# Performance work log

Measured on AMD Instinct MI355X. Metric: run time of the kernel, lower is better.

## Reference

```python
import jax, jax.numpy as jnp
import numpy as np

S = 4096
V = 50000
E = 512
H = 512
CE = 128
CH = 128
T = 50


def _lstm_dir(x, W_ih, W_hh, b, reverse):
    # x: [S, D]; PyTorch gate order i, f, g, o. b = b_ih + b_hh fused.
    gx = x @ W_ih.T + b  # [S, 4H] precomputed input contribution
    Hd = W_hh.shape[1]
    def step(carry, g_t):
        h, c = carry
        g = g_t + h @ W_hh.T
        i, f, gg, o = jnp.split(g, 4, axis=-1)
        c = jax.nn.sigmoid(f) * c + jax.nn.sigmoid(i) * jnp.tanh(gg)
        h = jax.nn.sigmoid(o) * jnp.tanh(c)
        return (h, c), h
    init = (jnp.zeros((Hd,), x.dtype), jnp.zeros((Hd,), x.dtype))
    _, hs = jax.lax.scan(step, init, gx, reverse=reverse)
    return hs  # [S, H]


def _bilstm(x, Wih_f, Whh_f, b_f, Wih_b, Whh_b, b_b):
    fwd = _lstm_dir(x, Wih_f, Whh_f, b_f, False)
    bwd = _lstm_dir(x, Wih_b, Whh_b, b_b, True)
    return jnp.concatenate([fwd, bwd], axis=-1)  # [S, 2H]


def _viterbi(emissions, start_t, end_t, trans):
    # emissions: [S, T]. Standard CRF Viterbi (torchcrf semantics).
    score0 = start_t + emissions[0]  # [T]
    def step(score, emit):
        m = score[:, None] + trans          # [T_prev, T_cur]
        bp = jnp.argmax(m, axis=0)          # best previous tag for each cur tag
        new_score = jnp.max(m, axis=0) + emit
        return new_score, bp
    final, bps = jax.lax.scan(step, score0, emissions[1:])  # bps: [S-1, T]
    final = final + end_t
    last = jnp.argmax(final)
    def back(tag, bp):
        prev = bp[tag]
        return prev, prev
    _, path_head = jax.lax.scan(back, last, bps, reverse=True)  # [S-1]
    return jnp.concatenate([path_head, last[None]])  # [S]


def setup_inputs() -> dict:
    key = jax.random.key(0)
    ks = jax.random.split(key, 20)
    s = 0.05
    inp = {
        'sentence': jax.random.randint(ks[0], (S,), 0, V),
        'char_sentence': jax.random.randint(ks[1], (S,), 0, V),
        'word_emb': jax.random.normal(ks[2], (V, E), jnp.float32) * s,
        'char_emb': jax.random.normal(ks[3], (V, CE), jnp.float32) * s,
        # char BiLSTM
        'cWih_f': jax.random.normal(ks[4], (4 * CH, CE), jnp.float32) * s,
        'cWhh_f': jax.random.normal(ks[5], (4 * CH, CH), jnp.float32) * s,
        'cb_f': jnp.zeros((4 * CH,), jnp.float32),
        'cWih_b': jax.random.normal(ks[6], (4 * CH, CE), jnp.float32) * s,
        'cWhh_b': jax.random.normal(ks[7], (4 * CH, CH), jnp.float32) * s,
        'cb_b': jnp.zeros((4 * CH,), jnp.float32),
        # word BiLSTM (input dim E + 2*CH)
        'wWih_f': jax.random.normal(ks[8], (4 * H, E + 2 * CH), jnp.float32) * s,
        'wWhh_f': jax.random.normal(ks[9], (4 * H, H), jnp.float32) * s,
        'wb_f': jnp.zeros((4 * H,), jnp.float32),
        'wWih_b': jax.random.normal(ks[10], (4 * H, E + 2 * CH), jnp.float32) * s,
        'wWhh_b': jax.random.normal(ks[11], (4 * H, H), jnp.float32) * s,
        'wb_b': jnp.zeros((4 * H,), jnp.float32),
        # hidden2tag
        'W_tag': jax.random.normal(ks[12], (T, 2 * H), jnp.float32) * s,
        'b_tag': jnp.zeros((T,), jnp.float32),
        # CRF params
        'start_t': jax.random.normal(ks[13], (T,), jnp.float32) * s,
        'end_t': jax.random.normal(ks[14], (T,), jnp.float32) * s,
        'trans': jax.random.normal(ks[15], (T, T), jnp.float32) * s,
    }
    return inp


def reference(sentence, char_sentence, word_emb, char_emb,
              cWih_f, cWhh_f, cb_f, cWih_b, cWhh_b, cb_b,
              wWih_f, wWhh_f, wb_f, wWih_b, wWhh_b, wb_b,
              W_tag, b_tag, start_t, end_t, trans):
    we = word_emb[sentence]          # [S, E]
    ce = char_emb[char_sentence]     # [S, CE]
    char_out = _bilstm(ce, cWih_f, cWhh_f, cb_f, cWih_b, cWhh_b, cb_b)  # [S, 2*CH]
    emb = jnp.concatenate([we, char_out], axis=-1)  # [S, E + 2*CH]
    lstm_out = _bilstm(emb, wWih_f, wWhh_f, wb_f, wWih_b, wWhh_b, wb_b)  # [S, 2H]
    tag_space = lstm_out @ W_tag.T + b_tag  # [S, T] emissions
    path = _viterbi(tag_space, start_t, end_t, trans)  # [S] int32 tags
    return path
```

## Files before the change

### kernel.cpp

```cpp
#include <hip/hip_runtime.h>
#include <math.h>

#define SQ   4096
#define EDIM 512
#define CEDIM 128
#define CHH  128
#define WH   512
#define NT   50

typedef unsigned long long ull;

__device__ __forceinline__ float sigf(float x) { return 1.0f / (1.0f + expf(-x)); }

#define PIN4(V) asm volatile("" : "+v"(V.x), "+v"(V.y), "+v"(V.z), "+v"(V.w));

__device__ __forceinline__ void ld8x_sc0(const ull* p, ull& q0, ull& q1, ull& q2,
                                         ull& q3, ull& q4, ull& q5, ull& q6, ull& q7) {
    asm volatile("global_load_dwordx2 %0, %8, off sc0\n\t"
                 "global_load_dwordx2 %1, %8, off offset:8 sc0\n\t"
                 "global_load_dwordx2 %2, %8, off offset:16 sc0\n\t"
                 "global_load_dwordx2 %3, %8, off offset:24 sc0\n\t"
                 "global_load_dwordx2 %4, %8, off offset:32 sc0\n\t"
                 "global_load_dwordx2 %5, %8, off offset:40 sc0\n\t"
                 "global_load_dwordx2 %6, %8, off offset:48 sc0\n\t"
                 "global_load_dwordx2 %7, %8, off offset:56 sc0\n\t"
                 "s_waitcnt vmcnt(0)"
                 : "=&v"(q0), "=&v"(q1), "=&v"(q2), "=&v"(q3),
                   "=&v"(q4), "=&v"(q5), "=&v"(q6), "=&v"(q7)
                 : "v"(p) : "memory");
}
__device__ __forceinline__ ull ld_mir(const ull* p) {
    return __hip_atomic_load(p, __ATOMIC_RELAXED, __HIP_MEMORY_SCOPE_AGENT);
}
__device__ __forceinline__ void st_plain8(ull* p, ull v) {
    asm volatile("global_store_dwordx2 %0, %1, off" :: "v"(p), "v"(v) : "memory");
}
__device__ __forceinline__ void st_mir(ull* p, ull v) {
    __hip_atomic_store(p, v, __ATOMIC_RELAXED, __HIP_MEMORY_SCOPE_AGENT);
}
__device__ __forceinline__ unsigned umin2(unsigned a, unsigned b) { return a < b ? a : b; }

#define FMA4(W, off) { float4 h4 = *(const float4*)&hc[off]; \
    a0 += W.x * h4.x; a1 += W.y * h4.y; a2 += W.z * h4.z; a3 += W.w * h4.w; }

#define CW(n) float4 w##n = wp[n]; PIN4(w##n)

__global__ __launch_bounds__(256) void k1_gather_cgx(
    const int* __restrict__ sent, const int* __restrict__ csent,
    const float* __restrict__ wemb, const float* __restrict__ cemb,
    const float* __restrict__ cWih_f, const float* __restrict__ cb_f,
    const float* __restrict__ cWih_b, const float* __restrict__ cb_b,
    float* __restrict__ we_g, float* __restrict__ cgx)
{
    const int tid = threadIdx.x;
    const int t0 = blockIdx.x * 16;
    __shared__ __align__(16) float ceL[16][128];
    __shared__ int sids[16], cids[16];
    if (tid < 16) sids[tid] = sent[t0 + tid];
    else if (tid < 32) cids[tid - 16] = csent[t0 + tid - 16];
    __syncthreads();
    {
        int f4 = tid;
        for (int q = 0; q < 2; ++q, f4 += 256) {
            int r = f4 >> 5, k4 = f4 & 31;
            float4 v = *(const float4*)&cemb[(size_t)cids[r] * CEDIM + k4 * 4];
            *(float4*)&ceL[r][k4 * 4] = v;
        }
    }
    {
        int f4 = tid;
        for (int q = 0; q < 8; ++q, f4 += 256) {
            int r = f4 >> 7, k4 = f4 & 127;
            float4 v = *(const float4*)&wemb[(size_t)sids[r] * EDIM + k4 * 4];
            *(float4*)&we_g[(size_t)(t0 + r) * EDIM + k4 * 4] = v;
        }
    }
    __syncthreads();
    for (int q = 0; q < 4; ++q) {
        int j = q * 256 + tid;
        int d = j >> 9, r = j & 511;
        const float* Wih = d ? cWih_b : cWih_f;
        const float* cb = d ? cb_b : cb_f;
        float b = cb[r];
        float acc[16];
#pragma unroll
        for (int tt = 0; tt < 16; ++tt) acc[tt] = b;
        for (int k4 = 0; k4 < 32; ++k4) {
            float4 wv = *(const float4*)&Wih[r * CEDIM + k4 * 4];
#pragma unroll
            for (int tt = 0; tt < 16; ++tt) {
                acc[tt] += wv.x * ceL[tt][k4 * 4 + 0] + wv.y * ceL[tt][k4 * 4 + 1]
                         + wv.z * ceL[tt][k4 * 4 + 2] + wv.w * ceL[tt][k4 * 4 + 3];
            }
        }
#pragma unroll
        for (int tt = 0; tt < 16; ++tt)
            cgx[((size_t)d * SQ + (t0 + tt)) * 512 + r] = acc[tt];
    }
}

__global__ __launch_bounds__(512, 2) void k2_charlstm_gemm(
    const float* __restrict__ cWhh_f, const float* __restrict__ cWhh_b,
    const float* __restrict__ cgx, float* __restrict__ cho,
    const float* __restrict__ we_g,
    const float* __restrict__ wWih_f, const float* __restrict__ wb_f,
    const float* __restrict__ wWih_b, const float* __restrict__ wb_b,
    float* __restrict__ wgx)
{
    const int tid = threadIdx.x;
    __shared__ __align__(16) float At[32][68];
    __shared__ __align__(16) float Bt[32][128];
    __shared__ __align__(16) float hstC[128];
    __shared__ float gb[512];

    if (blockIdx.x < 2) {
        const int dir = blockIdx.x;
        const float* Whh = dir ? cWhh_b : cWhh_f;
        const int row = tid;
        const float4* wp = (const float4*)&Whh[(size_t)row * CHH];
        CW(0)  CW(1)  CW(2)  CW(3)  CW(4)  CW(5)  CW(6)  CW(7)
        CW(8)  CW(9)  CW(10) CW(11) CW(12) CW(13) CW(14) CW(15)
        CW(16) CW(17) CW(18) CW(19) CW(20) CW(21) CW(22) CW(23)
        CW(24) CW(25) CW(26) CW(27) CW(28) CW(29) CW(30) CW(31)

        const float* gxc = cgx + (size_t)dir * SQ * 512;
        float cst = 0.f;
        float gxp0 = gxc[(size_t)(dir ? (SQ - 1) : 0) * 512 + row];
        float gxp1 = gxc[(size_t)(dir ? (SQ - 2) : 1) * 512 + row];
        if (tid < 32) *(float4*)&hstC[tid * 4] = make_float4(0, 0, 0, 0);
        __syncthreads();
        for (int t = 0; t < SQ; ++t) {
            const int x = dir ? (SQ - 1 - t) : t;
            float gxv = gxp0;
            gxp0 = gxp1;
            if (t + 2 < SQ) {
                const int x2 = dir ? (SQ - 3 - t) : (t + 2);
                gxp1 = gxc[(size_t)x2 * 512 + row];
            }
            float a0 = 0.f, a1 = 0.f, a2 = 0.f, a3 = 0.f;
            const float* hc = hstC;
            FMA4(w0, 0)    FMA4(w1, 4)    FMA4(w2, 8)    FMA4(w3, 12)
            FMA4(w4, 16)   FMA4(w5, 20)   FMA4(w6, 24)   FMA4(w7, 28)
            FMA4(w8, 32)   FMA4(w9, 36)   FMA4(w10, 40)  FMA4(w11, 44)
            FMA4(w12, 48)  FMA4(w13, 52)  FMA4(w14, 56)  FMA4(w15, 60)
            FMA4(w16, 64)  FMA4(w17, 68)  FMA4(w18, 72)  FMA4(w19, 76)
            FMA4(w20, 80)  FMA4(w21, 84)  FMA4(w22, 88)  FMA4(w23, 92)
            FMA4(w24, 96)  FMA4(w25, 100) FMA4(w26, 104) FMA4(w27, 108)
            FMA4(w28, 112) FMA4(w29, 116) FMA4(w30, 120) FMA4(w31, 124)
            gb[row] = (a0 + a1) + (a2 + a3) + gxv;
            __syncthreads();
            if (tid < 128) {
                float siv = gb[tid], sfv = gb[128 + tid];
                float sgv = gb[256 + tid], sov = gb[384 + tid];
                float iv = sigf(siv), fv = sigf(sfv), ov = sigf(sov);
                float yg = sigf(sgv + sgv);
                float gv = yg + yg - 1.f;
                cst = fv * cst + iv * gv;
                float ts = sigf(cst + cst);
                float h = ov * (ts + ts - 1.f);
                hstC[tid] = h;
                cho[(size_t)x * 256 + dir * CHH + tid] = h;
            }
            __syncthreads();
        }
        return;
    }
    const int tile = blockIdx.x - 2;
    const int dir = tile >> 10;
    const int rem = tile & 1023;
    const int mb = rem >> 4;
    const int nb = rem & 15;
    const float* Wih = dir ? wWih_b : wWih_f;
    const float* wb = dir ? wb_b : wb_f;
    float* C = wgx + (size_t)dir * SQ * 2048;
    const int tm = tid >> 5, tn = tid & 31;
    float acc[4][4];
#pragma unroll
    for (int i = 0; i < 4; ++i)
#pragma unroll
        for (int jj = 0; jj < 4; ++jj) acc[i][jj] = 0.f;
    for (int kb = 0; kb < 16; ++kb) {
        {
            int rowm = tid >> 3, k4 = tid & 7;
            float4 v = *(const float4*)&we_g[(size_t)(mb * 64 + rowm) * EDIM + kb * 32 + k4 * 4];
            At[k4 * 4 + 0][rowm] = v.x; At[k4 * 4 + 1][rowm] = v.y;
            At[k4 * 4 + 2][rowm] = v.z; At[k4 * 4 + 3][rowm] = v.w;
        }
#pragma unroll
        for (int q = 0; q < 2; ++q) {
            int f4 = q * 512 + tid;
            int rr = f4 >> 3, k4 = f4 & 7;
            float4 v = *(const float4*)&Wih[(size_t)(nb * 128 + rr) * 768 + kb * 32 + k4 * 4];
            Bt[k4 * 4 + 0][rr] = v.x; Bt[k4 * 4 + 1][rr] = v.y;
            Bt[k4 * 4 + 2][rr] = v.z; Bt[k4 * 4 + 3][rr] = v.w;
        }
        __syncthreads();
#pragma unroll
        for (int kk = 0; kk < 32; ++kk) {
            float4 a4 = *(const float4*)&At[kk][tm * 4];
            float4 b4 = *(const float4*)&Bt[kk][tn * 4];
            acc[0][0] += a4.x * b4.x; acc[0][1] += a4.x * b4.y; acc[0][2] += a4.x * b4.z; acc[0][3] += a4.x * b4.w;
            acc[1][0] += a4.y * b4.x; acc[1][1] += a4.y * b4.y; acc[1][2] += a4.y * b4.z; acc[1][3] += a4.y * b4.w;
            acc[2][0] += a4.z * b4.x; acc[2][1] += a4.z * b4.y; acc[2][2] += a4.z * b4.z; acc[2][3] += a4.z * b4.w;
            acc[3][0] += a4.w * b4.x; acc[3][1] += a4.w * b4.y; acc[3][2] += a4.w * b4.z; acc[3][3] += a4.w * b4.w;
        }
        __syncthreads();
    }
    float4 wbv = *(const float4*)&wb[nb * 128 + tn * 4];
#pragma unroll
    for (int i = 0; i < 4; ++i) {
        float4 o;
        o.x = acc[i][0] + wbv.x; o.y = acc[i][1] + wbv.y;
        o.z = acc[i][2] + wbv.z; o.w = acc[i][3] + wbv.w;
        *(float4*)&C[(size_t)(mb * 64 + tm * 4 + i) * 2048 + nb * 128 + tn * 4] = o;
    }
}

__global__ __launch_bounds__(512, 2) void k3_gemm_char(
    const float* __restrict__ cho,
    const float* __restrict__ wWih_f, const float* __restrict__ wWih_b,
    float* __restrict__ wgx)
{
    const int tid = threadIdx.x;
    const int tile = blockIdx.x;
    const int dir = tile >> 10;
    const int rem = tile & 1023;
    const int mb = rem >> 4, nb = rem & 15;
    const float* Wih = dir ? wWih_b : wWih_f;
    float* C = wgx + (size_t)dir * SQ * 2048;
    __shared__ __align__(16) float At[32][68];
    __shared__ __align__(16) float Bt[32][128];
    const int tm = tid >> 5, tn = tid & 31;
    float acc[4][4];
#pragma unroll
    for (int i = 0; i < 4; ++i)
#pragma unroll
        for (int jj = 0; jj < 4; ++jj) acc[i][jj] = 0.f;
    for (int kb = 0; kb < 8; ++kb) {
        {
            int rowm = tid >> 3, k4 = tid & 7;
            float4 v = *(const float4*)&cho[(size_t)(mb * 64 + rowm) * 256 + kb * 32 + k4 * 4];
            At[k4 * 4 + 0][rowm] = v.x; At[k4 * 4 + 1][rowm] = v.y;
            At[k4 * 4 + 2][rowm] = v.z; At[k4 * 4 + 3][rowm] = v.w;
        }
#pragma unroll
        for (int q = 0; q < 2; ++q) {
            int f4 = q * 512 + tid;
            int rr = f4 >> 3, k4 = f4 & 7;
            float4 v = *(const float4*)&Wih[(size_t)(nb * 128 + rr) * 768 + 512 + kb * 32 + k4 * 4];
            Bt[k4 * 4 + 0][rr] = v.x; Bt[k4 * 4 + 1][rr] = v.y;
            Bt[k4 * 4 + 2][rr] = v.z; Bt[k4 * 4 + 3][rr] = v.w;
        }
        __syncthreads();
#pragma unroll
        for (int kk = 0; kk < 32; ++kk) {
            float4 a4 = *(const float4*)&At[kk][tm * 4];
            float4 b4 = *(const float4*)&Bt[kk][tn * 4];
            acc[0][0] += a4.x * b4.x; acc[0][1] += a4.x * b4.y; acc[0][2] += a4.x * b4.z; acc[0][3] += a4.x * b4.w;
            acc[1][0] += a4.y * b4.x; acc[1][1] += a4.y * b4.y; acc[1][2] += a4.y * b4.z; acc[1][3] += a4.y * b4.w;
            acc[2][0] += a4.z * b4.x; acc[2][1] += a4.z * b4.y; acc[2][2] += a4.z * b4.z; acc[2][3] += a4.z * b4.w;
            acc[3][0] += a4.w * b4.x; acc[3][1] += a4.w * b4.y; acc[3][2] += a4.w * b4.z; acc[3][3] += a4.w * b4.w;
        }
        __syncthreads();
    }
#pragma unroll
    for (int i = 0; i < 4; ++i) {
        float* cp = &C[(size_t)(mb * 64 + tm * 4 + i) * 2048 + nb * 128 + tn * 4];
        float4 o = *(float4*)cp;
        o.x += acc[i][0]; o.y += acc[i][1]; o.z += acc[i][2]; o.w += acc[i][3];
        *(float4*)cp = o;
    }
}

__global__ __launch_bounds__(1024, 4) void k4_word_lstm(
    const float* __restrict__ wWhh_f, const float* __restrict__ wWhh_b,
    const float* __restrict__ wgx, float* __restrict__ lstm, ull* __restrict__ pairs)
{
    const int res = blockIdx.x & 7;
    if (res > 1) return;
    const int dir = res;
    const int wid = blockIdx.x >> 3;
    const int tid = threadIdx.x;
    const int k = tid >> 6;
    const int r = tid & 63;
    const int g = r >> 4, u = r & 15;
    const float* Whh = dir ? wWhh_b : wWhh_f;
    const int G = g * WH + wid * 16 + u;
    const float4* wp = (const float4*)&Whh[(size_t)G * WH + k * 32];
    float4 w0 = wp[0], w1 = wp[1], w2 = wp[2], w3 = wp[3];
    float4 w4 = wp[4], w5 = wp[5], w6 = wp[6], w7 = wp[7];
    PIN4(w0) PIN4(w1) PIN4(w2) PIN4(w3) PIN4(w4) PIN4(w5) PIN4(w6) PIN4(w7)

    __shared__ __align__(16) float hst[512];
    __shared__ float part[16][65];

    ull* wpf = pairs;
    ull* wpm = pairs + 2048;
    const float* gx = wgx + (size_t)dir * SQ * 2048;
    float cst = 0.f;
    int useFast = 1, alive = 1;
    for (int t = 0; t < SQ; ++t) {
        const int x = dir ? (SQ - 1 - t) : t;
        float gxv = 0.f;
        if (tid < 64)
            gxv = gx[(size_t)x * 2048 + (size_t)(tid >> 4) * 512 + wid * 16 + (tid & 15)];
        if (t == 0) {
            if (tid < 128) *(float4*)&hst[tid * 4] = make_float4(0, 0, 0, 0);
        } else if (tid < 64) {
            const size_t boff = ((size_t)((t - 1) & 1) * 2 + dir) * 512 + tid * 8;
            const ull* pf = wpf + boff;
            const ull* pm = wpm + boff;
            ull q0 = 0, q1 = 0, q2 = 0, q3 = 0, q4 = 0, q5 = 0, q6 = 0, q7 = 0;
            int spins = 0;
            while (alive) {
                if (useFast) {
                    ld8x_sc0(pf, q0, q1, q2, q3, q4, q5, q6, q7);
                } else {
                    q0 = ld_mir(pm + 0); q1 = ld_mir(pm + 1);
                    q2 = ld_mir(pm + 2); q3 = ld_mir(pm + 3);
                    q4 = ld_mir(pm + 4); q5 = ld_mir(pm + 5);
                    q6 = ld_mir(pm + 6); q7 = ld_mir(pm + 7);
                }
                unsigned tm = umin2(umin2(umin2((unsigned)(q0 >> 32), (unsigned)(q1 >> 32)),
                                          umin2((unsigned)(q2 >> 32), (unsigned)(q3 >> 32))),
                                    umin2(umin2((unsigned)(q4 >> 32), (unsigned)(q5 >> 32)),
                                          umin2((unsigned)(q6 >> 32), (unsigned)(q7 >> 32))));
                if (__all(tm >= (unsigned)t)) break;
                ++spins;
                if (useFast && spins > 2048) { useFast = 0; spins = 0; }
                if (!useFast && spins > (1 << 20)) alive = 0;
                __builtin_amdgcn_s_sleep(1);
            }
            float* hd = &hst[tid * 8];
            hd[0] = __uint_as_float((unsigned)q0); hd[1] = __uint_as_float((unsigned)q1);
            hd[2] = __uint_as_float((unsigned)q2); hd[3] = __uint_as_float((unsigned)q3);
            hd[4] = __uint_as_float((unsigned)q4); hd[5] = __uint_as_float((unsigned)q5);
            hd[6] = __uint_as_float((unsigned)q6); hd[7] = __uint_as_float((unsigned)q7);
        }
        __syncthreads();
        float a0 = 0.f, a1 = 0.f, a2 = 0.f, a3 = 0.f;
        const float* hc = &hst[k * 32];
        FMA4(w0, 0)  FMA4(w1, 4)  FMA4(w2, 8)  FMA4(w3, 12)
        FMA4(w4, 16) FMA4(w5, 20) FMA4(w6, 24) FMA4(w7, 28)
        part[k][r] = (a0 + a1) + (a2 + a3);
        __syncthreads();
        if (tid < 64) {
            float s = gxv;
#pragma unroll
            for (int kk = 0; kk < 16; ++kk) s += part[kk][tid];
            const bool isg = ((tid >> 4) == 2);
            float y = sigf(isg ? (s + s) : s);
            float val = isg ? (y + y - 1.f) : y;
            float fv = __shfl(val, 16 + (tid & 15));
            float gv = __shfl(val, 32 + (tid & 15));
            float ov = __shfl(val, 48 + (tid & 15));
            if (tid < 16) {
                cst = fv * cst + val * gv;
                float ts = sigf(cst + cst);
                float h = ov * (ts + ts - 1.f);
                const int unit = wid * 16 + tid;
                lstm[(size_t)x * 1024 + dir * WH + unit] = h;
                ull q = ((ull)(unsigned)(t + 1) << 32) | (ull)__float_as_uint(h);
                const size_t poff = ((size_t)(t & 1) * 2 + dir) * 512 + unit;
                st_plain8(wpf + poff, q);
                st_mir(wpm + poff, q);
            }
        }
    }
}

__global__ __launch_bounds__(64) void k5_emis(
    const float* __restrict__ lstm, const float* __restrict__ Wtag,
    const float* __restrict__ btag, float* __restrict__ emis)
{
    const int t = blockIdx.x, tid = threadIdx.x;
    __shared__ __align__(16) float rowL[1024];
#pragma unroll
    for (int q = 0; q < 4; ++q) {
        int f4 = q * 64 + tid;
        *(float4*)&rowL[f4 * 4] = *(const float4*)&lstm[(size_t)t * 1024 + f4 * 4];
    }
    __syncthreads();
    if (tid < NT) {
        float a0 = 0.f, a1 = 0.f, a2 = 0.f, a3 = 0.f;
        const float* wr = Wtag + (size_t)tid * 1024;
        for (int k4 = 0; k4 < 256; ++k4) {
            float4 wv = *(const float4*)&wr[k4 * 4];
            a0 += wv.x * rowL[k4 * 4 + 0];
            a1 += wv.y * rowL[k4 * 4 + 1];
            a2 += wv.z * rowL[k4 * 4 + 2];
            a3 += wv.w * rowL[k4 * 4 + 3];
        }
        emis[(size_t)t * NT + tid] = btag[tid] + (a0 + a1) + (a2 + a3);
    }
}

__global__ __launch_bounds__(256) void k6a_viterbi(
    const float* __restrict__ emis, const float* __restrict__ start_t,
    const float* __restrict__ end_t, const float* __restrict__ trans,
    unsigned char* __restrict__ bpb, int* __restrict__ last)
{
    const int tid = threadIdx.x;
    const int g = tid >> 6, c = tid & 63;
    __shared__ float sc[64];
    __shared__ float pbest[4][64];
    __shared__ int pbp[4][64];
    const int p0 = g * 13;
    float tr[13];
#pragma unroll
    for (int i = 0; i < 13; ++i) {
        int p = p0 + i;
        tr[i] = (c < NT && p < NT) ? trans[p * NT + c] : -1e30f;
    }
    if (tid < 64) sc[tid] = (tid < NT) ? (start_t[tid] + emis[tid]) : -1e30f;
    __syncthreads();
    for (int t = 1; t < SQ; ++t) {
        float best = -1e30f; int bp = 0;
#pragma unroll
        for (int i = 0; i < 13; ++i) {
            float v = sc[p0 + i] + tr[i];
            if (v > best) { best = v; bp = p0 + i; }
        }
        pbest[g][c] = best; pbp[g][c] = bp;
        __syncthreads();
        if (tid < NT) {
            float b = pbest[0][tid]; int bb = pbp[0][tid];
#pragma unroll
            for (int gg = 1; gg < 4; ++gg) {
                float v = pbest[gg][tid];
                if (v > b) { b = v; bb = pbp[gg][tid]; }
            }
            bpb[(size_t)t * NT + tid] = (unsigned char)bb;
            sc[tid] = b + emis[(size_t)t * NT + tid];
        }
        __syncthreads();
    }
    if (tid == 0) {
        float b = -1e30f; int bi = 0;
        for (int cc = 0; cc < NT; ++cc) {
            float v = sc[cc] + end_t[cc];
            if (v > b) { b = v; bi = cc; }
        }
        *last = bi;
    }
}

__global__ __launch_bounds__(64) void k6b_maps(
    const unsigned char* __restrict__ bpb, int* __restrict__ map_)
{
    const int k = blockIdx.x;
    const int e = threadIdx.x;
    if (k == 0 || e >= NT) return;
    int tag = e;
    for (int i = 63; i >= 0; --i) {
        int t = k * 64 + i;
        tag = bpb[(size_t)t * NT + tag];
    }
    map_[k * NT + e] = tag;
}

__global__ __launch_bounds__(64) void k6c_backtrack(
    const unsigned char* __restrict__ bpb, const int* __restrict__ map_,
    const int* __restrict__ last, int* __restrict__ path)
{
    __shared__ int B[64];
    if (threadIdx.x == 0) {
        int tag = *last;
        B[63] = tag;
        for (int k = 63; k >= 1; --k) {
            tag = map_[k * NT + tag];
            B[k - 1] = tag;
        }
    }
    __syncthreads();
    const int k = threadIdx.x;
    int tag = B[k];
    for (int i = 63; i >= 0; --i) {
        int t = k * 64 + i;
        path[t] = tag;
        if (t >= 1) tag = bpb[(size_t)t * NT + tag];
    }
}

extern "C" void kernel_launch(void* const* d_in, const int* in_sizes, int n_in,
                              void* d_out, int out_size, void* d_ws, size_t ws_size,
                              hipStream_t stream)
{
    const int* sent = (const int*)d_in[0];
    const int* csent = (const int*)d_in[1];
    const float* wemb = (const float*)d_in[2];
    const float* cemb = (const float*)d_in[3];
    const float* cWih_f = (const float*)d_in[4];
    const float* cWhh_f = (const float*)d_in[5];
    const float* cb_f = (const float*)d_in[6];
    const float* cWih_b = (const float*)d_in[7];
    const float* cWhh_b = (const float*)d_in[8];
    const float* cb_b = (const float*)d_in[9];
    const float* wWih_f = (const float*)d_in[10];
    const float* wWhh_f = (const float*)d_in[11];
    const float* wb_f = (const float*)d_in[12];
    const float* wWih_b = (const float*)d_in[13];
    const float* wWhh_b = (const float*)d_in[14];
    const float* wb_b = (const float*)d_in[15];
    const float* Wtag = (const float*)d_in[16];
    const float* btag = (const float*)d_in[17];
    const float* start_t = (const float*)d_in[18];
    const float* end_t = (const float*)d_in[19];
    const float* trans = (const float*)d_in[20];
    int* path = (int*)d_out;

    float* ws = (float*)d_ws;
    float* we_g = ws;
    float* cgx  = we_g + (size_t)SQ * EDIM;
    float* cho  = cgx + (size_t)2 * SQ * 512;
    float* wgx  = cho + (size_t)SQ * 256;
    float* lstm = wgx + (size_t)2 * SQ * 2048;
    float* emis = lstm + (size_t)SQ * 1024;
    ull* pairs  = (ull*)(emis + (size_t)SQ * NT);
    int* map_   = (int*)(pairs + 5120);
    int* lastp  = map_ + 64 * NT;
    unsigned char* bpb = (unsigned char*)(lastp + 4);

    (void)hipMemsetAsync(pairs, 0, 5120 * sizeof(ull), stream);

    k1_gather_cgx<<<SQ / 16, 256, 0, stream>>>(sent, csent, wemb, cemb,
                                               cWih_f, cb_f, cWih_b, cb_b, we_g, cgx);
    k2_charlstm_gemm<<<2 + 2048, 512, 0, stream>>>(cWhh_f, cWhh_b, cgx, cho, we_g,
                                                   wWih_f, wb_f, wWih_b, wb_b, wgx);
    k3_gemm_char<<<2048, 512, 0, stream>>>(cho, wWih_f, wWih_b, wgx);
    k4_word_lstm<<<256, 1024, 0, stream>>>(wWhh_f, wWhh_b, wgx, lstm, pairs);
    k5_emis<<<SQ, 64, 0, stream>>>(lstm, Wtag, btag, emis);
    k6a_viterbi<<<1, 256, 0, stream>>>(emis, start_t, end_t, trans, bpb, lastp);
    k6b_maps<<<64, 64, 0, stream>>>(bpb, map_);
    k6c_backtrack<<<1, 64, 0, stream>>>(bpb, map_, lastp, path);
}
```

Before: 16.61 ms.

## Split char LSTM and word input GEMM into separate kernels

Splits the fused kernel, where two blocks ran the sequential char BiLSTM while the other blocks computed the word-embedding input GEMM, into two kernels launched back to back on the same stream. The GEMM kernel now uses 1024 threads per block, with each thread producing a 4x2 output tile instead of 4x4. The intent is presumably to stop the LSTM blocks' register and occupancy needs from constraining the GEMM. The risk is that the long serial char LSTM and the GEMM no longer overlap, and the smaller per-thread tile lowers arithmetic intensity per LDS read.

Result: slower. 17.04 ms (+2.6%).

```diff
diff --git a/kernel.cpp b/kernel.cpp
--- a/kernel.cpp
+++ b/kernel.cpp
@@ -13,6 +13,7 @@
 __device__ __forceinline__ float sigf(float x) { return 1.0f / (1.0f + expf(-x)); }
 
 #define PIN4(V) asm volatile("" : "+v"(V.x), "+v"(V.y), "+v"(V.z), "+v"(V.w));
+#define CW(n) float4 w##n = wp[n]; PIN4(w##n)
 
 __device__ __forceinline__ void ld8x_sc0(const ull* p, ull& q0, ull& q1, ull& q2,
                                          ull& q3, ull& q4, ull& q5, ull& q6, ull& q7) {
@@ -43,8 +44,6 @@
 #define FMA4(W, off) { float4 h4 = *(const float4*)&hc[off]; \
     a0 += W.x * h4.x; a1 += W.y * h4.y; a2 += W.z * h4.z; a3 += W.w * h4.w; }
 
-#define CW(n) float4 w##n = wp[n]; PIN4(w##n)
-
 __global__ __launch_bounds__(256) void k1_gather_cgx(
     const int* __restrict__ sent, const int* __restrict__ csent,
     const float* __restrict__ wemb, const float* __restrict__ cemb,
@@ -99,9 +98,66 @@
     }
 }
 
-__global__ __launch_bounds__(512, 2) void k2_charlstm_gemm(
+__global__ __launch_bounds__(512, 1) void k2a_charlstm(
     const float* __restrict__ cWhh_f, const float* __restrict__ cWhh_b,
-    const float* __restrict__ cgx, float* __restrict__ cho,
+    const float* __restrict__ cgx, float* __restrict__ cho)
+{
+    const int tid = threadIdx.x;
+    __shared__ __align__(16) float hstC[128];
+    __shared__ float gb[512];
+
+    const int dir = blockIdx.x;
+    const float* Whh = dir ? cWhh_b : cWhh_f;
+    const int row = tid;
+    const float4* wp = (const float4*)&Whh[(size_t)row * CHH];
+    CW(0)  CW(1)  CW(2)  CW(3)  CW(4)  CW(5)  CW(6)  CW(7)
+    CW(8)  CW(9)  CW(10) CW(11) CW(12) CW(13) CW(14) CW(15)
+    CW(16) CW(17) CW(18) CW(19) CW(20) CW(21) CW(22) CW(23)
+    CW(24) CW(25) CW(26) CW(27) CW(28) CW(29) CW(30) CW(31)
+
+    const float* gxc = cgx + (size_t)dir * SQ * 512;
+    float cst = 0.f;
+    float gxp0 = gxc[(size_t)(dir ? (SQ - 1) : 0) * 512 + row];
+    float gxp1 = gxc[(size_t)(dir ? (SQ - 2) : 1) * 512 + row];
+    if (tid < 32) *(float4*)&hstC[tid * 4] = make_float4(0, 0, 0, 0);
+    __syncthreads();
+    for (int t = 0; t < SQ; ++t) {
+        const int x = dir ? (SQ - 1 - t) : t;
+        float gxv = gxp0;
+        gxp0 = gxp1;
+        if (t + 2 < SQ) {
+            const int x2 = dir ? (SQ - 3 - t) : (t + 2);
+            gxp1 = gxc[(size_t)x2 * 512 + row];
+        }
+        float a0 = 0.f, a1 = 0.f, a2 = 0.f, a3 = 0.f;
+        const float* hc = hstC;
+        FMA4(w0, 0)    FMA4(w1, 4)    FMA4(w2, 8)    FMA4(w3, 12)
+        FMA4(w4, 16)   FMA4(w5, 20)   FMA4(w6, 24)   FMA4(w7, 28)
+        FMA4(w8, 32)   FMA4(w9, 36)   FMA4(w10, 40)  FMA4(w11, 44)
+        FMA4(w12, 48)  FMA4(w13, 52)  FMA4(w14, 56)  FMA4(w15, 60)
+        FMA4(w16, 64)  FMA4(w17, 68)  FMA4(w18, 72)  FMA4(w19, 76)
+        FMA4(w20, 80)  FMA4(w21, 84)  FMA4(w22, 88)  FMA4(w23, 92)
+        FMA4(w24, 96)  FMA4(w25, 100) FMA4(w26, 104) FMA4(w27, 108)
+        FMA4(w28, 112) FMA4(w29, 116) FMA4(w30, 120) FMA4(w31, 124)
+        gb[row] = (a0 + a1) + (a2 + a3) + gxv;
+        __syncthreads();
+        if (tid < 128) {
+            float siv = gb[tid], sfv = gb[128 + tid];
+            float sgv = gb[256 + tid], sov = gb[384 + tid];
+            float iv = sigf(siv), fv = sigf(sfv), ov = sigf(sov);
+            float yg = sigf(sgv + sgv);
+            float gv = yg + yg - 1.f;
+            cst = fv * cst + iv * gv;
+            float ts = sigf(cst + cst);
+            float h = ov * (ts + ts - 1.f);
+            hstC[tid] = h;
+            cho[(size_t)x * 256 + dir * CHH + tid] = h;
+        }
+        __syncthreads();
+    }
+}
+
+__global__ __launch_bounds__(1024, 4) void k2b_gemm(
     const float* __restrict__ we_g,
     const float* __restrict__ wWih_f, const float* __restrict__ wb_f,
     const float* __restrict__ wWih_b, const float* __restrict__ wb_b,
@@ -110,62 +166,7 @@
     const int tid = threadIdx.x;
     __shared__ __align__(16) float At[32][68];
     __shared__ __align__(16) float Bt[32][128];
-    __shared__ __align__(16) float hstC[128];
-    __shared__ float gb[512];
-
-    if (blockIdx.x < 2) {
-        const int dir = blockIdx.x;
-        const float* Whh = dir ? cWhh_b : cWhh_f;
-        const int row = tid;
-        const float4* wp = (const float4*)&Whh[(size_t)row * CHH];
-        CW(0)  CW(1)  CW(2)  CW(3)  CW(4)  CW(5)  CW(6)  CW(7)
-        CW(8)  CW(9)  CW(10) CW(11) CW(12) CW(13) CW(14) CW(15)
-        CW(16) CW(17) CW(18) CW(19) CW(20) CW(21) CW(22) CW(23)
-        CW(24) CW(25) CW(26) CW(27) CW(28) CW(29) CW(30) CW(31)
-
-        const float* gxc = cgx + (size_t)dir * SQ * 512;
-        float cst = 0.f;
-        float gxp0 = gxc[(size_t)(dir ? (SQ - 1) : 0) * 512 + row];
-        float gxp1 = gxc[(size_t)(dir ? (SQ - 2) : 1) * 512 + row];
-        if (tid < 32) *(float4*)&hstC[tid * 4] = make_float4(0, 0, 0, 0);
-        __syncthreads();
-        for (int t = 0; t < SQ; ++t) {
-            const int x = dir ? (SQ - 1 - t) : t;
-            float gxv = gxp0;
-            gxp0 = gxp1;
-            if (t + 2 < SQ) {
-                const int x2 = dir ? (SQ - 3 - t) : (t + 2);
-                gxp1 = gxc[(size_t)x2 * 512 + row];
-            }
-            float a0 = 0.f, a1 = 0.f, a2 = 0.f, a3 = 0.f;
-            const float* hc = hstC;
-            FMA4(w0, 0)    FMA4(w1, 4)    FMA4(w2, 8)    FMA4(w3, 12)
-            FMA4(w4, 16)   FMA4(w5, 20)   FMA4(w6, 24)   FMA4(w7, 28)
-            FMA4(w8, 32)   FMA4(w9, 36)   FMA4(w10, 40)  FMA4(w11, 44)
-            FMA4(w12, 48)  FMA4(w13, 52)  FMA4(w14, 56)  FMA4(w15, 60)
-            FMA4(w16, 64)  FMA4(w17, 68)  FMA4(w18, 72)  FMA4(w19, 76)
-            FMA4(w20, 80)  FMA4(w21, 84)  FMA4(w22, 88)  FMA4(w23, 92)
-            FMA4(w24, 96)  FMA4(w25, 100) FMA4(w26, 104) FMA4(w27, 108)
-            FMA4(w28, 112) FMA4(w29, 116) FMA4(w30, 120) FMA4(w31, 124)
-            gb[row] = (a0 + a1) + (a2 + a3) + gxv;
-            __syncthreads();
-            if (tid < 128) {
-                float siv = gb[tid], sfv = gb[128 + tid];
-                float sgv = gb[256 + tid], sov = gb[384 + tid];
-                float iv = sigf(siv), fv = sigf(sfv), ov = sigf(sov);
-                float yg = sigf(sgv + sgv);
-                float gv = yg + yg - 1.f;
-                cst = fv * cst + iv * gv;
-                float ts = sigf(cst + cst);
-                float h = ov * (ts + ts - 1.f);
-                hstC[tid] = h;
-                cho[(size_t)x * 256 + dir * CHH + tid] = h;
-            }
-            __syncthreads();
-        }
-        return;
-    }
-    const int tile = blockIdx.x - 2;
+    const int tile = blockIdx.x;
     const int dir = tile >> 10;
     const int rem = tile & 1023;
     const int mb = rem >> 4;
@@ -173,23 +174,19 @@
     const float* Wih = dir ? wWih_b : wWih_f;
     const float* wb = dir ? wb_b : wb_f;
     float* C = wgx + (size_t)dir * SQ * 2048;
-    const int tm = tid >> 5, tn = tid & 31;
-    float acc[4][4];
-#pragma unroll
-    for (int i = 0; i < 4; ++i)
-#pragma unroll
-        for (int jj = 0; jj < 4; ++jj) acc[i][jj] = 0.f;
+    const int tm = tid >> 6, tn = tid & 63;
+    float acc[4][2];
+#pragma unroll
+    for (int i = 0; i < 4; ++i) { acc[i][0] = 0.f; acc[i][1] = 0.f; }
     for (int kb = 0; kb < 16; ++kb) {
-        {
+        if (tid < 512) {
             int rowm = tid >> 3, k4 = tid & 7;
             float4 v = *(const float4*)&we_g[(size_t)(mb * 64 + rowm) * EDIM + kb * 32 + k4 * 4];
             At[k4 * 4 + 0][rowm] = v.x; At[k4 * 4 + 1][rowm] = v.y;
             At[k4 * 4 + 2][rowm] = v.z; At[k4 * 4 + 3][rowm] = v.w;
         }
-#pragma unroll
-        for (int q = 0; q < 2; ++q) {
-            int f4 = q * 512 + tid;
-            int rr = f4 >> 3, k4 = f4 & 7;
+        {
+            int rr = tid >> 3, k4 = tid & 7;
             float4 v = *(const float4*)&Wih[(size_t)(nb * 128 + rr) * 768 + kb * 32 + k4 * 4];
             Bt[k4 * 4 + 0][rr] = v.x; Bt[k4 * 4 + 1][rr] = v.y;
             Bt[k4 * 4 + 2][rr] = v.z; Bt[k4 * 4 + 3][rr] = v.w;
@@ -198,21 +195,20 @@
 #pragma unroll
         for (int kk = 0; kk < 32; ++kk) {
             float4 a4 = *(const float4*)&At[kk][tm * 4];
-            float4 b4 = *(const float4*)&Bt[kk][tn * 4];
-            acc[0][0] += a4.x * b4.x; acc[0][1] += a4.x * b4.y; acc[0][2] += a4.x * b4.z; acc[0][3] += a4.x * b4.w;
-            acc[1][0] += a4.y * b4.x; acc[1][1] += a4.y * b4.y; acc[1][2] += a4.y * b4.z; acc[1][3] += a4.y * b4.w;
-            acc[2][0] += a4.z * b4.x; acc[2][1] += a4.z * b4.y; acc[2][2] += a4.z * b4.z; acc[2][3] += a4.z * b4.w;
-            acc[3][0] += a4.w * b4.x; acc[3][1] += a4.w * b4.y; acc[3][2] += a4.w * b4.z; acc[3][3] += a4.w * b4.w;
-        }
-        __syncthreads();
-    }
-    float4 wbv = *(const float4*)&wb[nb * 128 + tn * 4];
+            float2 b2 = *(const float2*)&Bt[kk][tn * 2];
+            acc[0][0] += a4.x * b2.x; acc[0][1] += a4.x * b2.y;
+            acc[1][0] += a4.y * b2.x; acc[1][1] += a4.y * b2.y;
+            acc[2][0] += a4.z * b2.x; acc[2][1] += a4.z * b2.y;
+            acc[3][0] += a4.w * b2.x; acc[3][1] += a4.w * b2.y;
+        }
+        __syncthreads();
+    }
+    float2 wbv = *(const float2*)&wb[nb * 128 + tn * 2];
 #pragma unroll
     for (int i = 0; i < 4; ++i) {
-        float4 o;
+        float2 o;
         o.x = acc[i][0] + wbv.x; o.y = acc[i][1] + wbv.y;
-        o.z = acc[i][2] + wbv.z; o.w = acc[i][3] + wbv.w;
-        *(float4*)&C[(size_t)(mb * 64 + tm * 4 + i) * 2048 + nb * 128 + tn * 4] = o;
+        *(float2*)&C[(size_t)(mb * 64 + tm * 4 + i) * 2048 + nb * 128 + tn * 2] = o;
     }
 }
 
@@ -525,8 +521,8 @@
 
     k1_gather_cgx<<<SQ / 16, 256, 0, stream>>>(sent, csent, wemb, cemb,
                                                cWih_f, cb_f, cWih_b, cb_b, we_g, cgx);
-    k2_charlstm_gemm<<<2 + 2048, 512, 0, stream>>>(cWhh_f, cWhh_b, cgx, cho, we_g,
-                                                   wWih_f, wb_f, wWih_b, wb_b, wgx);
+    k2a_charlstm<<<2, 512, 0, stream>>>(cWhh_f, cWhh_b, cgx, cho);
+    k2b_gemm<<<2048, 1024, 0, stream>>>(we_g, wWih_f, wb_f, wWih_b, wb_b, wgx);
     k3_gemm_char<<<2048, 512, 0, stream>>>(cho, wWih_f, wWih_b, wgx);
     k4_word_lstm<<<256, 1024, 0, stream>>>(wWhh_f, wWhh_b, wgx, lstm, pairs);
     k5_emis<<<SQ, 64, 0, stream>>>(lstm, Wtag, btag, emis);
```
